# Kernel optimization log

Hardware: AMD Instinct MI355X
Metric: run time of the kernel (lower is better)

Reference implementation:

```python
import itertools
import jax, jax.numpy as jnp
import numpy as np

GAMMA = 1.0

def setup_inputs() -> dict:
    key = jax.random.key(0)
    ks = jax.random.split(key, 11)
    B, T, NP, NG, J, H = 16, 32, 8, 4, 14, 256
    return {
        'hor_heatmap': jax.random.normal(ks[0], (B, T, 1, H, H), jnp.float32),
        'hor_offset': jax.random.normal(ks[1], (B, T, NP, 2), jnp.float32),
        'hor_bsize': jax.random.normal(ks[2], (B, T, NP, 4), jnp.float32),
        'hor_center': jax.random.normal(ks[3], (B, T, NP, 2), jnp.float32),
        'scores': jax.random.uniform(ks[4], (B, T, NP), jnp.float32),
        'x_pose3d': jax.random.normal(ks[5], (B, T, NP, J, 3), jnp.float32),
        'gt_heatmap': jax.random.normal(ks[6], (B, T, H, H), jnp.float32),
        'gt_hor_boxes_wh': jax.random.normal(ks[7], (B, T, NG, 4), jnp.float32),
        'gt_hor_offset': jax.random.normal(ks[8], (B, T, NG, 2), jnp.float32),
        'gt_hor_center': jax.random.normal(ks[9], (B, T, NG, 2), jnp.float32),
        'gt_pose3d': jax.random.normal(ks[10], (B, T, NG, J, 3), jnp.float32),
    }

def _make_perms(num_pred, num_gt):
    # all injective assignments of each gt column to a distinct pred row
    return np.asarray(list(itertools.permutations(range(num_pred), num_gt)), dtype=np.int32)

def _match(cost, perms):
    # cost: [NP, NG]; perms: [P, NG] static. Exact linear_sum_assignment by enumeration.
    ng = cost.shape[1]
    totals = cost[perms, jnp.arange(ng)].sum(-1)  # [P]
    return perms[jnp.argmin(totals)]              # rows matched to cols 0..NG-1

def reference(hor_heatmap, hor_offset, hor_bsize, hor_center, scores, x_pose3d,
              gt_heatmap, gt_hor_boxes_wh, gt_hor_offset, gt_hor_center, gt_pose3d):
    B, T, NP, _ = hor_center.shape
    NG = gt_hor_center.shape[2]
    J = x_pose3d.shape[3]
    BT = B * T
    perms = jnp.asarray(_make_perms(NP, NG))

    # center loss: MSE mean over full heatmaps
    center_loss = jnp.mean((hor_heatmap[:, :, 0] - gt_heatmap) ** 2)

    # --- Hungarian box/offset losses, vmapped over (b,t) ---
    def per_bt_box(pc, gc, sc, po, go, ps, gs):
        # cost[i,j] = -score[i] + ||pc_i - gc_j||
        C = jnp.linalg.norm(pc[:, None] - gc[None], axis=-1) - sc[:, None]  # [NP,NG]
        rows = _match(C, perms)                                             # [NG]
        off = jnp.mean(jnp.abs(po[rows] - go), axis=-1).sum()   # L1 mean per pair, summed
        size = jnp.mean(jnp.abs(ps[rows] - gs), axis=-1).sum()
        return off, size

    flat = lambda x: x.reshape((BT,) + x.shape[2:])
    offs, sizes = jax.vmap(per_bt_box)(
        flat(hor_center), flat(gt_hor_center), flat(scores),
        flat(hor_offset), flat(gt_hor_offset), flat(hor_bsize), flat(gt_hor_boxes_wh))
    total_offset_loss = offs.sum() / BT
    total_size_loss = sizes.sum() / BT

    # --- Hungarian pose loss ---
    def per_bt_pose(pp, gp):
        d = pp[:, None] - gp[None]                       # [NP,NG,J,3]
        C = jnp.sqrt(jnp.sum(d * d, axis=(-1, -2)))      # Frobenius norm cost
        rows = _match(C, perms)
        return jnp.sum((pp[rows] - gp) ** 2)             # MSE(sum) per pair, summed

    pose_loss = jax.vmap(per_bt_pose)(flat(x_pose3d), flat(gt_pose3d)).sum() / (BT * NP * J)

    detection_loss = center_loss + total_offset_loss + total_size_loss
    return GAMMA * detection_loss + pose_loss
```

## Files before the change

### kernel.cpp

```cpp
#include <hip/hip_runtime.h>

#define BT      512
#define NP      8
#define NG      4
#define JNT     14
#define NCENTER 33554432
#define NBLK_CENTER 4096
#define WOFF    NBLK_CENTER


__global__ __launch_bounds__(256) void main_kernel(
    const float* __restrict__ hm,
    const float* __restrict__ hor_offset,
    const float* __restrict__ hor_bsize,
    const float* __restrict__ hor_center,
    const float* __restrict__ scores,
    const float* __restrict__ x_pose3d,
    const float* __restrict__ gt_hm,
    const float* __restrict__ gt_wh,
    const float* __restrict__ gt_off,
    const float* __restrict__ gt_center,
    const float* __restrict__ gt_pose,
    float* __restrict__ ws,
    int use_atomics)
{
    __shared__ float sC[32];
    __shared__ float sCp[32];
    __shared__ float sv[8];
    __shared__ int   sp[8];

    const int blk = blockIdx.x;
    const int tid = threadIdx.x;

    if (blk < NBLK_CENTER) {
        const float4* a = (const float4*)hm;
        const float4* b = (const float4*)gt_hm;
        const int gsz  = NBLK_CENTER * 256;
        const int base = blk * 256 + tid;
        float s = 0.0f;
        #pragma unroll 4
        for (int k = 0; k < 8; k++) {
            const int i = base + k * gsz;
            float4 x = a[i];
            float4 y = b[i];
            float d0 = x.x - y.x, d1 = x.y - y.y, d2 = x.z - y.z, d3 = x.w - y.w;
            s += d0 * d0 + d1 * d1 + d2 * d2 + d3 * d3;
        }
        #pragma unroll
        for (int o = 32; o > 0; o >>= 1) s += __shfl_down(s, o);
        const int lane = tid & 63, w = tid >> 6;
        if (lane == 0) sv[w] = s;
        __syncthreads();
        if (tid == 0) {
            float tot = sv[0] + sv[1] + sv[2] + sv[3];
            if (use_atomics) atomicAdd(&ws[0], tot);
            else             ws[blk] = tot;
        }
        return;
    }

    const int c = blk - NBLK_CENTER;
    const float* pc = hor_center + c * (NP * 2);
    const float* gc = gt_center  + c * (NG * 2);
    const float* sc = scores     + c * NP;
    const float* po = hor_offset + c * (NP * 2);
    const float* go = gt_off     + c * (NG * 2);
    const float* ps = hor_bsize  + c * (NP * 4);
    const float* gs = gt_wh      + c * (NG * 4);
    const float* pp = x_pose3d   + c * (NP * JNT * 3);
    const float* gp = gt_pose    + c * (NG * JNT * 3);

    if (tid < 32) {
        const int i = tid >> 2;
        const int j = tid & 3;
        float dx = pc[i * 2 + 0] - gc[j * 2 + 0];
        float dy = pc[i * 2 + 1] - gc[j * 2 + 1];
        sC[i * 4 + j] = sqrtf(dx * dx + dy * dy) - sc[i];
        float acc = 0.0f;
        const float* ai = pp + i * (JNT * 3);
        const float* gj = gp + j * (JNT * 3);
        #pragma unroll
        for (int k = 0; k < JNT * 3; k++) {
            float d = ai[k] - gj[k];
            acc += d * d;
        }
        sCp[i * 4 + j] = sqrtf(acc);
    }
    __syncthreads();

    float bv = 1e30f, bv2 = 1e30f;
    int bp = 0x7fffffff, bp2 = 0x7fffffff;
    for (int p = tid; p < 4096; p += 256) {
        const int i0 = (p >> 9) & 7, i1 = (p >> 6) & 7, i2 = (p >> 3) & 7, i3 = p & 7;
        if (i0 == i1 || i0 == i2 || i0 == i3 || i1 == i2 || i1 == i3 || i2 == i3) continue;
        float t  = sC [i0 * 4 + 0] + sC [i1 * 4 + 1] + sC [i2 * 4 + 2] + sC [i3 * 4 + 3];
        float t2 = sCp[i0 * 4 + 0] + sCp[i1 * 4 + 1] + sCp[i2 * 4 + 2] + sCp[i3 * 4 + 3];
        if (t  < bv)  { bv  = t;  bp  = p; }
        if (t2 < bv2) { bv2 = t2; bp2 = p; }
    }
    #pragma unroll
    for (int o = 32; o > 0; o >>= 1) {
        float v2 = __shfl_down(bv, o);  int p2 = __shfl_down(bp, o);
        if (v2 < bv  || (v2 == bv  && p2 < bp))  { bv  = v2; bp  = p2; }
        float w2 = __shfl_down(bv2, o); int q2 = __shfl_down(bp2, o);
        if (w2 < bv2 || (w2 == bv2 && q2 < bp2)) { bv2 = w2; bp2 = q2; }
    }
    const int lane = tid & 63, w = tid >> 6;
    if (lane == 0) { sv[w] = bv; sp[w] = bp; sv[4 + w] = bv2; sp[4 + w] = bp2; }
    __syncthreads();

    if (tid == 0) {
        for (int k = 1; k < 4; k++) {
            if (sv[k] < sv[0] || (sv[k] == sv[0] && sp[k] < sp[0])) { sv[0] = sv[k]; sp[0] = sp[k]; }
            if (sv[4 + k] < sv[4] || (sv[4 + k] == sv[4] && sp[4 + k] < sp[4])) { sv[4] = sv[4 + k]; sp[4] = sp[4 + k]; }
        }
        const int pb = sp[0];
        const int pq = sp[4];
        float off = 0.0f, size = 0.0f, pose = 0.0f;
        #pragma unroll
        for (int jj = 0; jj < 4; jj++) {
            const int r = (pb >> (9 - 3 * jj)) & 7;
            off += 0.5f * (fabsf(po[r * 2 + 0] - go[jj * 2 + 0]) +
                           fabsf(po[r * 2 + 1] - go[jj * 2 + 1]));
            size += 0.25f * (fabsf(ps[r * 4 + 0] - gs[jj * 4 + 0]) +
                             fabsf(ps[r * 4 + 1] - gs[jj * 4 + 1]) +
                             fabsf(ps[r * 4 + 2] - gs[jj * 4 + 2]) +
                             fabsf(ps[r * 4 + 3] - gs[jj * 4 + 3]));
            const int r2 = (pq >> (9 - 3 * jj)) & 7;
            const float* ai = pp + r2 * (JNT * 3);
            const float* gj = gp + jj * (JNT * 3);
            for (int k = 0; k < JNT * 3; k++) {
                float d = ai[k] - gj[k];
                pose += d * d;
            }
        }
        if (use_atomics) {
            atomicAdd(&ws[1], off);
            atomicAdd(&ws[2], size);
            atomicAdd(&ws[3], pose);
        } else {
            float* slot = ws + WOFF + c * 4;
            slot[0] = off;
            slot[1] = size;
            slot[2] = pose;
        }
    }
}

__global__ __launch_bounds__(256) void final_partials_kernel(
    const float* __restrict__ ws, float* __restrict__ out)
{
    __shared__ float red[16];
    const int tid = threadIdx.x;
    float s0 = 0.0f, s1 = 0.0f, s2 = 0.0f, s3 = 0.0f;
    for (int i = tid; i < NBLK_CENTER; i += 256) s0 += ws[i];
    for (int c = tid; c < BT; c += 256) {
        const float* slot = ws + WOFF + c * 4;
        s1 += slot[0];
        s2 += slot[1];
        s3 += slot[2];
    }
    #pragma unroll
    for (int o = 32; o > 0; o >>= 1) {
        s0 += __shfl_down(s0, o);
        s1 += __shfl_down(s1, o);
        s2 += __shfl_down(s2, o);
        s3 += __shfl_down(s3, o);
    }
    const int lane = tid & 63, w = tid >> 6;
    if (lane == 0) { red[w] = s0; red[4 + w] = s1; red[8 + w] = s2; red[12 + w] = s3; }
    __syncthreads();
    if (tid == 0) {
        s0 = red[0] + red[1] + red[2] + red[3];
        s1 = red[4] + red[5] + red[6] + red[7];
        s2 = red[8] + red[9] + red[10] + red[11];
        s3 = red[12] + red[13] + red[14] + red[15];
        out[0] = s0 * (1.0f / (float)NCENTER)
               + (s1 + s2) * (1.0f / (float)BT)
               + s3 * (1.0f / (float)(BT * NP * JNT));
    }
}


__global__ void init_ws_kernel(float* __restrict__ ws) {
    if (threadIdx.x < 4) ws[threadIdx.x] = 0.0f;
}

__global__ void final_atomic_kernel(const float* __restrict__ ws, float* __restrict__ out) {
    out[0] = ws[0] * (1.0f / (float)NCENTER)
           + (ws[1] + ws[2]) * (1.0f / (float)BT)
           + ws[3] * (1.0f / (float)(BT * NP * JNT));
}

extern "C" void kernel_launch(void* const* d_in, const int* in_sizes, int n_in,
                              void* d_out, int out_size, void* d_ws, size_t ws_size,
                              hipStream_t stream) {
    const float* hm         = (const float*)d_in[0];
    const float* hor_offset = (const float*)d_in[1];
    const float* hor_bsize  = (const float*)d_in[2];
    const float* hor_center = (const float*)d_in[3];
    const float* scores     = (const float*)d_in[4];
    const float* x_pose3d   = (const float*)d_in[5];
    const float* gt_hm      = (const float*)d_in[6];
    const float* gt_wh      = (const float*)d_in[7];
    const float* gt_off     = (const float*)d_in[8];
    const float* gt_center  = (const float*)d_in[9];
    const float* gt_pose    = (const float*)d_in[10];
    float* ws  = (float*)d_ws;
    float* out = (float*)d_out;

    const size_t needed = (size_t)(NBLK_CENTER + 4 * BT) * sizeof(float);
    const int use_atomics = (ws_size < needed) ? 1 : 0;

    if (use_atomics) init_ws_kernel<<<1, 64, 0, stream>>>(ws);
    main_kernel<<<NBLK_CENTER + BT, 256, 0, stream>>>(
        hm, hor_offset, hor_bsize, hor_center, scores, x_pose3d,
        gt_hm, gt_wh, gt_off, gt_center, gt_pose, ws, use_atomics);
    if (use_atomics) final_atomic_kernel<<<1, 1, 0, stream>>>(ws, out);
    else             final_partials_kernel<<<1, 256, 0, stream>>>(ws, out);
}
```

Before: 308.6 us.

## Split center MSE and Hungarian matching into separate kernels, parallelize loss tail

Separates the fused kernel into a center-MSE streaming kernel, now 1024 blocks each handling 32 float4 pairs with two accumulators, and a Hungarian kernel launched before it. The Hungarian kernel stages its per-sample inputs in shared memory and packs both cost matrices into one float2 array. Its final loss evaluation is spread across a wavefront instead of running on a single thread, and the pre-scaled partials are merged into one slot. The intent is to shorten the serial tail of the matching blocks and give the bandwidth-bound reduction more memory parallelism per thread, at the cost of an extra kernel launch and fewer resident center blocks.

```diff
diff --git a/kernel.cpp b/kernel.cpp
--- a/kernel.cpp
+++ b/kernel.cpp
@@ -5,86 +5,102 @@
 #define NG      4
 #define JNT     14
 #define NCENTER 33554432
-#define NBLK_CENTER 4096
-#define WOFF    NBLK_CENTER
-
-
-__global__ __launch_bounds__(256) void main_kernel(
-    const float* __restrict__ hm,
+#define N4      8388608
+#define CBLK    1024
+#define CSTEP   (CBLK*256)
+#define HALF4   (N4/2)
+
+
+__global__ __launch_bounds__(256) void center_kernel(
+    const float* __restrict__ hm, const float* __restrict__ gt_hm,
+    float* __restrict__ ws, int use_atomics)
+{
+    __shared__ float sv[4];
+    const int tid = threadIdx.x;
+    const int base = blockIdx.x * 256 + tid;
+    const float4* a = (const float4*)hm;
+    const float4* b = (const float4*)gt_hm;
+    float s0 = 0.0f, s1 = 0.0f;
+    for (int k = 0; k < 16; k++) {
+        const int i = base + k * CSTEP;
+        float4 x0 = a[i];
+        float4 y0 = b[i];
+        float4 x1 = a[i + HALF4];
+        float4 y1 = b[i + HALF4];
+        float d0 = x0.x - y0.x, d1 = x0.y - y0.y, d2 = x0.z - y0.z, d3 = x0.w - y0.w;
+        s0 += d0 * d0 + d1 * d1 + d2 * d2 + d3 * d3;
+        float e0 = x1.x - y1.x, e1 = x1.y - y1.y, e2 = x1.z - y1.z, e3 = x1.w - y1.w;
+        s1 += e0 * e0 + e1 * e1 + e2 * e2 + e3 * e3;
+    }
+    float s = s0 + s1;
+    #pragma unroll
+    for (int o = 32; o > 0; o >>= 1) s += __shfl_down(s, o);
+    const int lane = tid & 63, w = tid >> 6;
+    if (lane == 0) sv[w] = s;
+    __syncthreads();
+    if (tid == 0) {
+        float tot = sv[0] + sv[1] + sv[2] + sv[3];
+        if (use_atomics) atomicAdd(&ws[0], tot);
+        else             ws[blockIdx.x] = tot;
+    }
+}
+
+__global__ __launch_bounds__(256) void hungarian_kernel(
     const float* __restrict__ hor_offset,
     const float* __restrict__ hor_bsize,
     const float* __restrict__ hor_center,
     const float* __restrict__ scores,
     const float* __restrict__ x_pose3d,
-    const float* __restrict__ gt_hm,
     const float* __restrict__ gt_wh,
     const float* __restrict__ gt_off,
     const float* __restrict__ gt_center,
     const float* __restrict__ gt_pose,
-    float* __restrict__ ws,
-    int use_atomics)
+    float* __restrict__ ws, int use_atomics)
 {
-    __shared__ float sC[32];
-    __shared__ float sCp[32];
+    __shared__ float sPP[NP * JNT * 3];
+    __shared__ float sGP[NG * JNT * 3];
+    __shared__ float sPO[NP * 2];
+    __shared__ float sGO[NG * 2];
+    __shared__ float sPS[NP * 4];
+    __shared__ float sGS[NG * 4];
+    __shared__ float sPC[NP * 2];
+    __shared__ float sGC[NG * 2];
+    __shared__ float sSC[NP];
+    __shared__ float2 sCC[NP * NG];
     __shared__ float sv[8];
-    __shared__ int   sp[8];
-
-    const int blk = blockIdx.x;
+    __shared__ int   spx[8];
+    __shared__ int   sBest[2];
+
+    const int c   = blockIdx.x;
     const int tid = threadIdx.x;
 
-    if (blk < NBLK_CENTER) {
-        const float4* a = (const float4*)hm;
-        const float4* b = (const float4*)gt_hm;
-        const int gsz  = NBLK_CENTER * 256;
-        const int base = blk * 256 + tid;
-        float s = 0.0f;
-        #pragma unroll 4
-        for (int k = 0; k < 8; k++) {
-            const int i = base + k * gsz;
-            float4 x = a[i];
-            float4 y = b[i];
-            float d0 = x.x - y.x, d1 = x.y - y.y, d2 = x.z - y.z, d3 = x.w - y.w;
-            s += d0 * d0 + d1 * d1 + d2 * d2 + d3 * d3;
-        }
-        #pragma unroll
-        for (int o = 32; o > 0; o >>= 1) s += __shfl_down(s, o);
-        const int lane = tid & 63, w = tid >> 6;
-        if (lane == 0) sv[w] = s;
-        __syncthreads();
-        if (tid == 0) {
-            float tot = sv[0] + sv[1] + sv[2] + sv[3];
-            if (use_atomics) atomicAdd(&ws[0], tot);
-            else             ws[blk] = tot;
-        }
-        return;
-    }
-
-    const int c = blk - NBLK_CENTER;
-    const float* pc = hor_center + c * (NP * 2);
-    const float* gc = gt_center  + c * (NG * 2);
-    const float* sc = scores     + c * NP;
-    const float* po = hor_offset + c * (NP * 2);
-    const float* go = gt_off     + c * (NG * 2);
-    const float* ps = hor_bsize  + c * (NP * 4);
-    const float* gs = gt_wh      + c * (NG * 4);
-    const float* pp = x_pose3d   + c * (NP * JNT * 3);
-    const float* gp = gt_pose    + c * (NG * JNT * 3);
+    {
+        const float* pp = x_pose3d  + c * (NP * JNT * 3);
+        const float* gp = gt_pose   + c * (NG * JNT * 3);
+        for (int k = tid; k < NP * JNT * 3; k += 256) sPP[k] = pp[k];
+        if (tid < NG * JNT * 3) sGP[tid] = gp[tid];
+        if (tid < NP * 2) sPO[tid] = hor_offset[c * NP * 2 + tid];
+        if (tid < NG * 2) sGO[tid] = gt_off[c * NG * 2 + tid];
+        if (tid < NP * 4) sPS[tid] = hor_bsize[c * NP * 4 + tid];
+        if (tid < NG * 4) sGS[tid] = gt_wh[c * NG * 4 + tid];
+        if (tid < NP * 2) sPC[tid] = hor_center[c * NP * 2 + tid];
+        if (tid < NG * 2) sGC[tid] = gt_center[c * NG * 2 + tid];
+        if (tid < NP)     sSC[tid] = scores[c * NP + tid];
+    }
+    __syncthreads();
 
     if (tid < 32) {
-        const int i = tid >> 2;
-        const int j = tid & 3;
-        float dx = pc[i * 2 + 0] - gc[j * 2 + 0];
-        float dy = pc[i * 2 + 1] - gc[j * 2 + 1];
-        sC[i * 4 + j] = sqrtf(dx * dx + dy * dy) - sc[i];
+        const int i = tid >> 2, j = tid & 3;
+        float dx = sPC[i * 2 + 0] - sGC[j * 2 + 0];
+        float dy = sPC[i * 2 + 1] - sGC[j * 2 + 1];
+        float box = sqrtf(dx * dx + dy * dy) - sSC[i];
         float acc = 0.0f;
-        const float* ai = pp + i * (JNT * 3);
-        const float* gj = gp + j * (JNT * 3);
         #pragma unroll
         for (int k = 0; k < JNT * 3; k++) {
-            float d = ai[k] - gj[k];
+            float d = sPP[i * (JNT * 3) + k] - sGP[j * (JNT * 3) + k];
             acc += d * d;
         }
-        sCp[i * 4 + j] = sqrtf(acc);
+        sCC[i * 4 + j] = make_float2(box, sqrtf(acc));
     }
     __syncthreads();
 
@@ -93,10 +109,11 @@
     for (int p = tid; p < 4096; p += 256) {
         const int i0 = (p >> 9) & 7, i1 = (p >> 6) & 7, i2 = (p >> 3) & 7, i3 = p & 7;
         if (i0 == i1 || i0 == i2 || i0 == i3 || i1 == i2 || i1 == i3 || i2 == i3) continue;
-        float t  = sC [i0 * 4 + 0] + sC [i1 * 4 + 1] + sC [i2 * 4 + 2] + sC [i3 * 4 + 3];
-        float t2 = sCp[i0 * 4 + 0] + sCp[i1 * 4 + 1] + sCp[i2 * 4 + 2] + sCp[i3 * 4 + 3];
-        if (t  < bv)  { bv  = t;  bp  = p; }
-        if (t2 < bv2) { bv2 = t2; bp2 = p; }
+        float2 t0 = sCC[i0 * 4 + 0], t1 = sCC[i1 * 4 + 1], t2 = sCC[i2 * 4 + 2], t3 = sCC[i3 * 4 + 3];
+        float t  = t0.x + t1.x + t2.x + t3.x;
+        float u  = t0.y + t1.y + t2.y + t3.y;
+        if (t < bv)  { bv  = t; bp  = p; }
+        if (u < bv2) { bv2 = u; bp2 = p; }
     }
     #pragma unroll
     for (int o = 32; o > 0; o >>= 1) {
@@ -106,43 +123,46 @@
         if (w2 < bv2 || (w2 == bv2 && q2 < bp2)) { bv2 = w2; bp2 = q2; }
     }
     const int lane = tid & 63, w = tid >> 6;
-    if (lane == 0) { sv[w] = bv; sp[w] = bp; sv[4 + w] = bv2; sp[4 + w] = bp2; }
-    __syncthreads();
-
+    if (lane == 0) { sv[w] = bv; spx[w] = bp; sv[4 + w] = bv2; spx[4 + w] = bp2; }
+    __syncthreads();
     if (tid == 0) {
         for (int k = 1; k < 4; k++) {
-            if (sv[k] < sv[0] || (sv[k] == sv[0] && sp[k] < sp[0])) { sv[0] = sv[k]; sp[0] = sp[k]; }
-            if (sv[4 + k] < sv[4] || (sv[4 + k] == sv[4] && sp[4 + k] < sp[4])) { sv[4] = sv[4 + k]; sp[4] = sp[4 + k]; }
-        }
-        const int pb = sp[0];
-        const int pq = sp[4];
-        float off = 0.0f, size = 0.0f, pose = 0.0f;
+            if (sv[k] < sv[0] || (sv[k] == sv[0] && spx[k] < spx[0])) { sv[0] = sv[k]; spx[0] = spx[k]; }
+            if (sv[4 + k] < sv[4] || (sv[4 + k] == sv[4] && spx[4 + k] < spx[4])) { sv[4] = sv[4 + k]; spx[4] = spx[4 + k]; }
+        }
+        sBest[0] = spx[0];
+        sBest[1] = spx[4];
+    }
+    __syncthreads();
+
+    if (tid < 64) {
+        const int pb = sBest[0], pq = sBest[1];
+        float contrib = 0.0f;
+        if (tid < JNT * 3) {
+            float acc = 0.0f;
+            #pragma unroll
+            for (int jj = 0; jj < 4; jj++) {
+                const int r2 = (pq >> (9 - 3 * jj)) & 7;
+                float d = sPP[r2 * (JNT * 3) + tid] - sGP[jj * (JNT * 3) + tid];
+                acc += d * d;
+            }
+            contrib += acc * (1.0f / (float)(BT * NP * JNT));
+        }
+        if (tid < 8) {
+            const int jj = tid >> 1, cm = tid & 1;
+            const int r = (pb >> (9 - 3 * jj)) & 7;
+            contrib += 0.5f * fabsf(sPO[r * 2 + cm] - sGO[jj * 2 + cm]) * (1.0f / (float)BT);
+        }
+        if (tid < 16) {
+            const int jj = tid >> 2, cm = tid & 3;
+            const int r = (pb >> (9 - 3 * jj)) & 7;
+            contrib += 0.25f * fabsf(sPS[r * 4 + cm] - sGS[jj * 4 + cm]) * (1.0f / (float)BT);
+        }
         #pragma unroll
-        for (int jj = 0; jj < 4; jj++) {
-            const int r = (pb >> (9 - 3 * jj)) & 7;
-            off += 0.5f * (fabsf(po[r * 2 + 0] - go[jj * 2 + 0]) +
-                           fabsf(po[r * 2 + 1] - go[jj * 2 + 1]));
-            size += 0.25f * (fabsf(ps[r * 4 + 0] - gs[jj * 4 + 0]) +
-                             fabsf(ps[r * 4 + 1] - gs[jj * 4 + 1]) +
-                             fabsf(ps[r * 4 + 2] - gs[jj * 4 + 2]) +
-                             fabsf(ps[r * 4 + 3] - gs[jj * 4 + 3]));
-            const int r2 = (pq >> (9 - 3 * jj)) & 7;
-            const float* ai = pp + r2 * (JNT * 3);
-            const float* gj = gp + jj * (JNT * 3);
-            for (int k = 0; k < JNT * 3; k++) {
-                float d = ai[k] - gj[k];
-                pose += d * d;
-            }
-        }
-        if (use_atomics) {
-            atomicAdd(&ws[1], off);
-            atomicAdd(&ws[2], size);
-            atomicAdd(&ws[3], pose);
-        } else {
-            float* slot = ws + WOFF + c * 4;
-            slot[0] = off;
-            slot[1] = size;
-            slot[2] = pose;
+        for (int o = 32; o > 0; o >>= 1) contrib += __shfl_down(contrib, o);
+        if (tid == 0) {
+            if (use_atomics) atomicAdd(&ws[1], contrib);
+            else             ws[CBLK + c] = contrib;
         }
     }
 }
@@ -150,46 +170,32 @@
 __global__ __launch_bounds__(256) void final_partials_kernel(
     const float* __restrict__ ws, float* __restrict__ out)
 {
-    __shared__ float red[16];
+    __shared__ float red[8];
     const int tid = threadIdx.x;
-    float s0 = 0.0f, s1 = 0.0f, s2 = 0.0f, s3 = 0.0f;
-    for (int i = tid; i < NBLK_CENTER; i += 256) s0 += ws[i];
-    for (int c = tid; c < BT; c += 256) {
-        const float* slot = ws + WOFF + c * 4;
-        s1 += slot[0];
-        s2 += slot[1];
-        s3 += slot[2];
-    }
+    float s0 = 0.0f, s1 = 0.0f;
+    for (int i = tid; i < CBLK; i += 256) s0 += ws[i];
+    for (int c = tid; c < BT; c += 256)   s1 += ws[CBLK + c];
     #pragma unroll
     for (int o = 32; o > 0; o >>= 1) {
         s0 += __shfl_down(s0, o);
         s1 += __shfl_down(s1, o);
-        s2 += __shfl_down(s2, o);
-        s3 += __shfl_down(s3, o);
     }
     const int lane = tid & 63, w = tid >> 6;
-    if (lane == 0) { red[w] = s0; red[4 + w] = s1; red[8 + w] = s2; red[12 + w] = s3; }
+    if (lane == 0) { red[w] = s0; red[4 + w] = s1; }
     __syncthreads();
     if (tid == 0) {
         s0 = red[0] + red[1] + red[2] + red[3];
         s1 = red[4] + red[5] + red[6] + red[7];
-        s2 = red[8] + red[9] + red[10] + red[11];
-        s3 = red[12] + red[13] + red[14] + red[15];
-        out[0] = s0 * (1.0f / (float)NCENTER)
-               + (s1 + s2) * (1.0f / (float)BT)
-               + s3 * (1.0f / (float)(BT * NP * JNT));
-    }
-}
-
+        out[0] = s0 * (1.0f / (float)NCENTER) + s1;
+    }
+}
 
 __global__ void init_ws_kernel(float* __restrict__ ws) {
-    if (threadIdx.x < 4) ws[threadIdx.x] = 0.0f;
+    if (threadIdx.x < 2) ws[threadIdx.x] = 0.0f;
 }
 
 __global__ void final_atomic_kernel(const float* __restrict__ ws, float* __restrict__ out) {
-    out[0] = ws[0] * (1.0f / (float)NCENTER)
-           + (ws[1] + ws[2]) * (1.0f / (float)BT)
-           + ws[3] * (1.0f / (float)(BT * NP * JNT));
+    out[0] = ws[0] * (1.0f / (float)NCENTER) + ws[1];
 }
 
 extern "C" void kernel_launch(void* const* d_in, const int* in_sizes, int n_in,
@@ -209,13 +215,14 @@
     float* ws  = (float*)d_ws;
     float* out = (float*)d_out;
 
-    const size_t needed = (size_t)(NBLK_CENTER + 4 * BT) * sizeof(float);
+    const size_t needed = (size_t)(CBLK + BT) * sizeof(float);
     const int use_atomics = (ws_size < needed) ? 1 : 0;
 
     if (use_atomics) init_ws_kernel<<<1, 64, 0, stream>>>(ws);
-    main_kernel<<<NBLK_CENTER + BT, 256, 0, stream>>>(
-        hm, hor_offset, hor_bsize, hor_center, scores, x_pose3d,
-        gt_hm, gt_wh, gt_off, gt_center, gt_pose, ws, use_atomics);
+    hungarian_kernel<<<BT, 256, 0, stream>>>(
+        hor_offset, hor_bsize, hor_center, scores, x_pose3d,
+        gt_wh, gt_off, gt_center, gt_pose, ws, use_atomics);
+    center_kernel<<<CBLK, 256, 0, stream>>>(hm, gt_hm, ws, use_atomics);
     if (use_atomics) final_atomic_kernel<<<1, 1, 0, stream>>>(ws, out);
     else             final_partials_kernel<<<1, 256, 0, stream>>>(ws, out);
 }
```

Result: no change. 305.4 us (-1.1%).
